# Performance work log

Hardware: AMD Instinct MI355X
Metric: run time of the kernel (lower is better)

The kernel has to match this reference:

```python
import jax, jax.numpy as jnp
import numpy as np

B, T, H, W = 1, 8, 48, 48
EMBED, HEADS = 512, 8
HD = EMBED // HEADS          # 64
KS = 3                       # spatial neighborhood kernel
ROT = HD // 3                # 21 -> 2*(21//2)=20 rotary dims per axis, 60 total
MAX_FREQ = 256.0
EPS = 1e-6


def _rms_norm(x, w):
    return x * jax.lax.rsqrt(jnp.mean(x * x, axis=-1, keepdims=True) + EPS) * w


def _axis_freqs(L, base):
    # freqs_for='pixel': positions in [-1, 1], freqs = linspace(1, max_freq/2)*pi
    pos = jnp.linspace(-1.0, 1.0, L)
    f = pos[:, None] * base[None, :]          # (L, ROT//2)
    return jnp.repeat(f, 2, axis=-1)          # (L, 2*(ROT//2)) interleaved pairs


def _axial_freqs(t, h, w):
    base = jnp.linspace(1.0, MAX_FREQ / 2.0, ROT // 2) * jnp.pi
    ft, fh, fw = _axis_freqs(t, base), _axis_freqs(h, base), _axis_freqs(w, base)
    d = ft.shape[-1]
    ft = jnp.broadcast_to(ft[:, None, None, :], (t, h, w, d))
    fh = jnp.broadcast_to(fh[None, :, None, :], (t, h, w, d))
    fw = jnp.broadcast_to(fw[None, None, :, :], (t, h, w, d))
    return jnp.concatenate([ft, fh, fw], axis=-1)  # (t, h, w, 3*d)


def _rotate_half(x):
    x1, x2 = x[..., ::2], x[..., 1::2]
    return jnp.stack((-x2, x1), axis=-1).reshape(x.shape)


def _apply_rope(freqs, x):
    r = freqs.shape[-1]
    xr, xt = x[..., :r], x[..., r:]
    xr = xr * jnp.cos(freqs) + _rotate_half(xr) * jnp.sin(freqs)
    return jnp.concatenate([xr, xt], axis=-1)


def reference(x, w_qkv, w_out, qnorm_w, knorm_w):
    b, t, h, w, c = x.shape
    # fused QKV: per-head contiguous [q|k|v] chunk of size 3*HD (matches
    # rearrange '(heads head_dim)' with head_dim = 3*HD, then tensor_split(3, -1))
    qkv = (x @ w_qkv.T).reshape(b, t, h, w, HEADS, 3 * HD)
    q, k, v = qkv[..., :HD], qkv[..., HD:2 * HD], qkv[..., 2 * HD:]
    q = _rms_norm(q, qnorm_w)
    k = _rms_norm(k, knorm_w)
    freqs = _axial_freqs(t, h, w)[:, :, :, None, :]  # broadcast over heads
    q = _apply_rope(freqs, q)
    k = _apply_rope(freqs, k)
    # neighborhood attention: full along t, clamped KSxKS window over (h, w)
    ih = jnp.clip(jnp.arange(h) - KS // 2, 0, h - KS)[:, None] + jnp.arange(KS)
    iw = jnp.clip(jnp.arange(w) - KS // 2, 0, w - KS)[:, None] + jnp.arange(KS)
    IH = ih[:, :, None, None]  # (h, KS, 1, 1)
    IW = iw[None, None, :, :]  # (1, 1, w, KS)
    kw = k[:, :, IH, IW]       # (b, t, h, KS, w, KS, heads, HD)
    vw = v[:, :, IH, IW]
    scores = jnp.einsum('btxynd,bsxiyjnd->bntxysij', q, kw) * (HD ** -0.5)
    attn = jax.nn.softmax(scores.reshape(b, HEADS, t, h, w, -1), axis=-1)
    attn = attn.reshape(scores.shape)
    out = jnp.einsum('bntxysij,bsxiyjnd->btxynd', attn, vw)
    out = out.reshape(b, t, h, w, c)
    return out @ w_out.T


def setup_inputs():
    key = jax.random.key(0)
    k1, k2, k3 = jax.random.split(key, 3)
    x = jax.random.normal(k1, (B, T, H, W, EMBED), jnp.float32)
    w_qkv = jax.random.normal(k2, (3 * EMBED, EMBED), jnp.float32) * 0.02
    w_out = jax.random.normal(k3, (EMBED, EMBED), jnp.float32) * 0.02
    qnorm_w = jnp.ones((HD,), jnp.float32)
    knorm_w = jnp.ones((HD,), jnp.float32)
    return dict(x=x, w_qkv=w_qkv, w_out=w_out, qnorm_w=qnorm_w, knorm_w=knorm_w)
```

## Files before the change

kernel.cpp:

```cpp
#include <hip/hip_runtime.h>
#include <hip/hip_bf16.h>
#include <math.h>

#define TOK 18432
#define EMB 512
#define NH 8
#define HD_ 64
#define HH 48
#define WW 48

typedef __attribute__((ext_vector_type(8))) __bf16 bf16x8;
typedef __attribute__((ext_vector_type(4))) float  f32x4;
typedef __attribute__((ext_vector_type(8))) unsigned short u16x8;

__device__ __forceinline__ ushort f2bf(float x) {
    __hip_bfloat16 b = __float2bfloat16(x);
    return *(ushort*)&b;
}
__device__ __forceinline__ float bf2f(ushort u) {
    __hip_bfloat16 b = *(__hip_bfloat16*)&u;
    return __bfloat162float(b);
}

__device__ __forceinline__ void gload16(const void* g, void* l) {
    __builtin_amdgcn_global_load_lds((const __attribute__((address_space(1))) void*)g,
                                     (__attribute__((address_space(3))) void*)l,
                                     16, 0, 0);
}

__device__ __forceinline__ f32x4 mfma_bf16(bf16x8 a, bf16x8 b, f32x4 c) {
    return __builtin_amdgcn_mfma_f32_16x16x32_bf16(a, b, c, 0, 0, 0);
}

__global__ __launch_bounds__(256) void init_misc(const float* __restrict__ x,
                                                 ushort* __restrict__ xhi,
                                                 const float* __restrict__ wq,
                                                 ushort* __restrict__ wqhi,
                                                 const float* __restrict__ wo,
                                                 ushort* __restrict__ wohi,
                                                 float2* __restrict__ tabs) {
    int b = blockIdx.x;
    if (b < 10240) {
        const float* src;
        ushort* dst;
        int i;
        if (b < 9216)      { src = x;  dst = xhi;  i = b * 256 + threadIdx.x; }
        else if (b < 9984) { src = wq; dst = wqhi; i = (b - 9216) * 256 + threadIdx.x; }
        else               { src = wo; dst = wohi; i = (b - 9984) * 256 + threadIdx.x; }
        float4 v = ((const float4*)src)[i];
        ushort4 h = {f2bf(v.x), f2bf(v.y), f2bf(v.z), f2bf(v.w)};
        ((ushort4*)dst)[i] = h;
    } else {
        int idx = (b - 10240) * 256 + threadIdx.x;
        if (idx >= 104 * 10) return;
        int row = idx / 10, j = idx % 10;
        float base = fmaf((float)j, 127.0f / 9.0f, 1.0f) * 3.14159265358979323846f;
        float pos;
        if (row < 8)       pos = fmaf((float)row,        2.0f / 7.0f,  -1.0f);
        else if (row < 56) pos = fmaf((float)(row - 8),  2.0f / 47.0f, -1.0f);
        else               pos = fmaf((float)(row - 56), 2.0f / 47.0f, -1.0f);
        float f = pos * base;
        tabs[idx] = make_float2(cosf(f), sinf(f));
    }
}

__global__ __launch_bounds__(256) void gemm_qkv(const ushort* __restrict__ Ah,
                                                const ushort* __restrict__ Bh,
                                                const float2* __restrict__ tabs,
                                                const float* __restrict__ qnw,
                                                const float* __restrict__ knw,
                                                ushort* __restrict__ qbf,
                                                ushort* __restrict__ kbf,
                                                ushort* __restrict__ vbf) {
    const int K = 512, nM = 12;
    __shared__ __align__(16) char smem[49152];
#define AS_(b) ((ushort*)(smem + (b) * 16384))
#define BS_(b) ((ushort*)(smem + (b) * 16384 + 8192))
    int nwg = gridDim.x;
    int bid = blockIdx.x;
    int cpx = nwg >> 3;
    int swz = (bid & 7) * cpx + (bid >> 3);
    int bm = (swz % nM) * 128, bn = (swz / nM) * 128;
    int tid = threadIdx.x;
    int lane = tid & 63, wave = tid >> 6;
    int wr = wave >> 1, wc = wave & 1;
    int fr = lane & 15, kg = lane >> 4;

    f32x4 acc[4][4];
#pragma unroll
    for (int m = 0; m < 4; ++m)
#pragma unroll
        for (int n = 0; n < 4; ++n) acc[m][n] = (f32x4){0.f, 0.f, 0.f, 0.f};

    auto stage = [&](int buf, int k0) {
#pragma unroll
        for (int it = 0; it < 2; ++it) {
            int f = it * 256 + tid;
            int row = f >> 2, ch = f & 3;
            int sl = ch ^ ((row >> 1) & 3);
            gload16(Ah + (size_t)(bm + row) * K + k0 + sl * 8, AS_(buf) + f * 8);
            gload16(Bh + (size_t)(bn + row) * K + k0 + sl * 8, BS_(buf) + f * 8);
        }
    };

    int nt = K >> 5;
    stage(0, 0);
    int cb = 0, nb = 1;
    int ksw = (kg ^ ((fr >> 1) & 3)) * 8;
    for (int t = 0; t < nt; ++t) {
        if (t + 1 < nt) {
            stage(nb, (t + 1) << 5);
            asm volatile("s_waitcnt vmcnt(4)" ::: "memory");
        } else {
            asm volatile("s_waitcnt vmcnt(0)" ::: "memory");
        }
        __builtin_amdgcn_s_barrier();
        __builtin_amdgcn_sched_barrier(0);
        const ushort* Bc = BS_(cb);
        const ushort* Ac = AS_(cb);
        bf16x8 bh[4];
#pragma unroll
        for (int n = 0; n < 4; ++n)
            bh[n] = *(const bf16x8*)&Bc[(wc * 64 + n * 16 + fr) * 32 + ksw];
#pragma unroll
        for (int m = 0; m < 4; ++m) {
            bf16x8 ah = *(const bf16x8*)&Ac[(wr * 64 + m * 16 + fr) * 32 + ksw];
#pragma unroll
            for (int n = 0; n < 4; ++n)
                acc[m][n] = mfma_bf16(ah, bh[n], acc[m][n]);
        }
        cb = (cb + 1 == 3) ? 0 : cb + 1;
        nb = (nb + 1 == 3) ? 0 : nb + 1;
    }
    __syncthreads();

    int g = (bm >> 6) + wr;
    int type = g % 3;
    int h = g / 3;
    ushort* obuf = (type == 0) ? qbf : (type == 1) ? kbf : vbf;
    float qsc = (type == 0) ? 0.125f : 1.0f;
    float4 wv[4];
    if (type < 2) {
        const float* wptr = type ? knw : qnw;
#pragma unroll
        for (int m = 0; m < 4; ++m)
            wv[m] = *(const float4*)&wptr[m * 16 + kg * 4];
    }
    char* tb = smem + wave * 5120;
    size_t obase = (size_t)h * TOK + bn + wc * 64;

#pragma unroll
    for (int hp = 0; hp < 2; ++hp) {
#pragma unroll
        for (int nn = 0; nn < 2; ++nn) {
            int n = hp * 2 + nn;
            int tk = bn + wc * 64 + n * 16 + fr;
            if (type == 2) {
#pragma unroll
                for (int m = 0; m < 4; ++m) {
                    ushort4 pk = {f2bf(acc[m][n][0]), f2bf(acc[m][n][1]),
                                  f2bf(acc[m][n][2]), f2bf(acc[m][n][3])};
                    *(ushort4*)(tb + (nn * 16 + fr) * 160 + (m * 16 + kg * 4) * 2) = pk;
                }
            } else {
                float s = 0.f;
#pragma unroll
                for (int m = 0; m < 4; ++m)
#pragma unroll
                    for (int i = 0; i < 4; ++i)
                        s = fmaf(acc[m][n][i], acc[m][n][i], s);
                s += __shfl_xor(s, 16);
                s += __shfl_xor(s, 32);
                float inv = rsqrtf(s * (1.0f / 64.0f) + 1e-6f);
                int t = tk / (HH * WW);
                int rem = tk % (HH * WW);
                int xx = rem / WW, yy = rem % WW;
#pragma unroll
                for (int m = 0; m < 4; ++m) {
                    float r[4];
                    const float* wm = (const float*)&wv[m];
#pragma unroll
                    for (int u = 0; u < 2; ++u) {
                        int dc0 = m * 16 + kg * 4 + 2 * u;
                        float xn0 = acc[m][n][2 * u]     * inv * wm[2 * u];
                        float xn1 = acc[m][n][2 * u + 1] * inv * wm[2 * u + 1];
                        if (dc0 < 60) {
                            int p = dc0 >> 1;
                            int tr = (p < 10) ? t * 10 + p
                                   : (p < 20) ? (8 + xx) * 10 + (p - 10)
                                              : (56 + yy) * 10 + (p - 20);
                            float2 cs = tabs[tr];
                            r[2 * u]     = fmaf(xn0, cs.x, -xn1 * cs.y);
                            r[2 * u + 1] = fmaf(xn1, cs.x,  xn0 * cs.y);
                        } else {
                            r[2 * u] = xn0;
                            r[2 * u + 1] = xn1;
                        }
                    }
                    ushort4 pk = {f2bf(r[0] * qsc), f2bf(r[1] * qsc),
                                  f2bf(r[2] * qsc), f2bf(r[3] * qsc)};
                    *(ushort4*)(tb + (nn * 16 + fr) * 160 + (m * 16 + kg * 4) * 2) = pk;
                }
            }
        }
#pragma unroll
        for (int j = 0; j < 4; ++j) {
            int row = j * 8 + (lane >> 3);
            int c16 = (lane & 7) * 16;
            u16x8 v = *(const u16x8*)(tb + row * 160 + c16);
            size_t tok = obase + hp * 32 + row;
            *(u16x8*)(obuf + tok * 64 + (lane & 7) * 8) = v;
        }
    }
#undef AS_
#undef BS_
}

__global__ __launch_bounds__(256) void gemm_out(const ushort* __restrict__ Ah,
                                                const ushort* __restrict__ Bh,
                                                float* __restrict__ C) {
    const int N = 512, K = 512, nbx = 4;
    __shared__ __align__(16) char smem[49152];
#define AS_(b) ((ushort*)(smem + (b) * 16384))
#define BS_(b) ((ushort*)(smem + (b) * 16384 + 8192))
    int nwg = gridDim.x;
    int bid = blockIdx.x;
    int cpx = nwg >> 3;
    int swz = (bid & 7) * cpx + (bid >> 3);
    int bm = (swz / nbx) * 128, bn = (swz % nbx) * 128;
    int tid = threadIdx.x;
    int lane = tid & 63, wave = tid >> 6;
    int wr = wave >> 1, wc = wave & 1;
    int fr = lane & 15, kg = lane >> 4;

    f32x4 acc[4][4];
#pragma unroll
    for (int m = 0; m < 4; ++m)
#pragma unroll
        for (int n = 0; n < 4; ++n) acc[m][n] = (f32x4){0.f, 0.f, 0.f, 0.f};

    auto stage = [&](int buf, int k0) {
#pragma unroll
        for (int it = 0; it < 2; ++it) {
            int f = it * 256 + tid;
            int row = f >> 2, ch = f & 3;
            int sl = ch ^ ((row >> 1) & 3);
            gload16(Ah + (size_t)(bm + row) * K + k0 + sl * 8, AS_(buf) + f * 8);
            gload16(Bh + (size_t)(bn + row) * K + k0 + sl * 8, BS_(buf) + f * 8);
        }
    };

    int nt = K >> 5;
    stage(0, 0);
    int cb = 0, nb = 1;
    int ksw = (kg ^ ((fr >> 1) & 3)) * 8;
    for (int t = 0; t < nt; ++t) {
        if (t + 1 < nt) {
            stage(nb, (t + 1) << 5);
            asm volatile("s_waitcnt vmcnt(4)" ::: "memory");
        } else {
            asm volatile("s_waitcnt vmcnt(0)" ::: "memory");
        }
        __builtin_amdgcn_s_barrier();
        __builtin_amdgcn_sched_barrier(0);
        const ushort* Bc = BS_(cb);
        const ushort* Ac = AS_(cb);
        bf16x8 bh[4];
#pragma unroll
        for (int n = 0; n < 4; ++n)
            bh[n] = *(const bf16x8*)&Bc[(wc * 64 + n * 16 + fr) * 32 + ksw];
#pragma unroll
        for (int m = 0; m < 4; ++m) {
            bf16x8 ah = *(const bf16x8*)&Ac[(wr * 64 + m * 16 + fr) * 32 + ksw];
#pragma unroll
            for (int n = 0; n < 4; ++n)
                acc[m][n] = mfma_bf16(ah, bh[n], acc[m][n]);
        }
        cb = (cb + 1 == 3) ? 0 : cb + 1;
        nb = (nb + 1 == 3) ? 0 : nb + 1;
    }
#pragma unroll
    for (int m = 0; m < 4; ++m) {
        int row0 = bm + wr * 64 + m * 16 + kg * 4;
#pragma unroll
        for (int n = 0; n < 4; ++n) {
            int col = bn + wc * 64 + n * 16 + fr;
#pragma unroll
            for (int i = 0; i < 4; ++i)
                C[(size_t)(row0 + i) * N + col] = acc[m][n][i];
        }
    }
#undef AS_
#undef BS_
}

__global__ __launch_bounds__(256) void attn_mfma(const ushort* __restrict__ qbf,
                                                 const ushort* __restrict__ kbf,
                                                 const ushort* __restrict__ vbf,
                                                 ushort* __restrict__ ohi) {
    __shared__ __align__(16) char smem[45056];
    constexpr int Q_OFF = 0;
    constexpr int K_OFF = 4096;
    constexpr int V_OFF = 20480;
    constexpr int P_OFF = 36864;

    int patch = blockIdx.x, head = blockIdx.y;
    int bi = patch / 24, bj = patch % 24;
    int x0 = bi * 2, y0 = bj * 2;
    int ubx = min(max(x0 - 1, 0), 44), uby = min(max(y0 - 1, 0), 44);
    int tid = threadIdx.x, lane = tid & 63, w = tid >> 6;
    int fr = lane & 15, kg = lane >> 4;
    size_t hbase = (size_t)head * TOK;

    {
        int f = tid;
        int row = f >> 3, sp = f & 7, sl = sp ^ (row & 7);
        int t = row >> 2, px = (row >> 1) & 1, py = row & 1;
        size_t tok = ((size_t)(t * HH + x0 + px)) * WW + (y0 + py);
        gload16(qbf + (hbase + tok) * 64 + sl * 8, smem + Q_OFF + f * 16);
    }
#pragma unroll
    for (int it = 0; it < 4; ++it) {
        int f = it * 256 + tid;
        int row = f >> 3, sp = f & 7, sl = sp ^ (row & 7);
        int s = row >> 4, ki = (row >> 2) & 3, kj = row & 3;
        size_t tok = ((size_t)(s * HH + ubx + ki)) * WW + (uby + kj);
        gload16(kbf + (hbase + tok) * 64 + sl * 8, smem + K_OFF + f * 16);
    }
#pragma unroll
    for (int it = 0; it < 2; ++it) {
        int u = it * 256 + tid;
        int sk = u >> 4, dg = u & 15;
        int s = sk >> 2, ki = sk & 3;
        ushort4 rv[4];
#pragma unroll
        for (int kj = 0; kj < 4; ++kj) {
            size_t tok = ((size_t)(s * HH + ubx + ki)) * WW + (uby + kj);
            rv[kj] = *(const ushort4*)(vbf + (hbase + tok) * 64 + dg * 4);
        }
        const ushort* rr = (const ushort*)rv;
#pragma unroll
        for (int dd = 0; dd < 4; ++dd) {
            int d = dg * 4 + dd;
            ushort4 val = {rr[dd], rr[4 + dd], rr[8 + dd], rr[12 + dd]};
            *(ushort4*)(smem + V_OFF + d * 256 + ((sk * 8) ^ ((d & 7) << 4))) = val;
        }
    }
    __syncthreads();

    if (w < 2) {
        int q = w * 16 + fr;
        bf16x8 qb[2];
#pragma unroll
        for (int ks = 0; ks < 2; ++ks)
            qb[ks] = *(const bf16x8*)(smem + Q_OFF + q * 128 +
                                      ((ks * 64 + kg * 16) ^ ((fr & 7) << 4)));
        f32x4 sc[8];
#pragma unroll
        for (int m = 0; m < 8; ++m) sc[m] = (f32x4){0.f, 0.f, 0.f, 0.f};
#pragma unroll
        for (int m = 0; m < 8; ++m)
#pragma unroll
            for (int ks = 0; ks < 2; ++ks) {
                bf16x8 a = *(const bf16x8*)(smem + K_OFF + (m * 16 + fr) * 128 +
                                            ((ks * 64 + kg * 16) ^ ((fr & 7) << 4)));
                sc[m] = mfma_bf16(a, qb[ks], sc[m]);
            }
        int xq = x0 + ((q >> 1) & 1), yq = y0 + (q & 1);
        int lox = min(max(xq - 1, 0), 45) - ubx;
        int loy = min(max(yq - 1, 0), 45) - uby;
        bool vki = ((unsigned)(kg - lox)) <= 2u;
        float mx = -1e30f;
        if (vki) {
#pragma unroll
            for (int m = 0; m < 8; ++m)
#pragma unroll
                for (int i = 0; i < 4; ++i)
                    if (((unsigned)(i - loy)) <= 2u) mx = fmaxf(mx, sc[m][i]);
        }
        mx = fmaxf(mx, __shfl_xor(mx, 16));
        mx = fmaxf(mx, __shfl_xor(mx, 32));
        float sum = 0.f;
#pragma unroll
        for (int m = 0; m < 8; ++m)
#pragma unroll
            for (int i = 0; i < 4; ++i) {
                bool v = vki && (((unsigned)(i - loy)) <= 2u);
                float e = v ? __expf(sc[m][i] - mx) : 0.f;
                sc[m][i] = e;
                sum += e;
            }
        sum += __shfl_xor(sum, 16);
        sum += __shfl_xor(sum, 32);
        float inv = 1.0f / sum;
#pragma unroll
        for (int m = 0; m < 8; ++m) {
            ushort4 pk = {f2bf(sc[m][0] * inv), f2bf(sc[m][1] * inv),
                          f2bf(sc[m][2] * inv), f2bf(sc[m][3] * inv)};
            *(ushort4*)(smem + P_OFF + q * 256 +
                        ((m * 32 + kg * 8) ^ ((q & 7) << 4))) = pk;
        }
    }
    __syncthreads();

    f32x4 ov[2];
    ov[0] = (f32x4){0.f, 0.f, 0.f, 0.f};
    ov[1] = (f32x4){0.f, 0.f, 0.f, 0.f};
#pragma unroll
    for (int kb = 0; kb < 4; ++kb) {
        bf16x8 a = *(const bf16x8*)(smem + V_OFF + (w * 16 + fr) * 256 +
                                    ((kb * 64 + kg * 16) ^ ((fr & 7) << 4)));
#pragma unroll
        for (int nt2 = 0; nt2 < 2; ++nt2) {
            bf16x8 b = *(const bf16x8*)(smem + P_OFF + (nt2 * 16 + fr) * 256 +
                                        ((kb * 64 + kg * 16) ^ ((fr & 7) << 4)));
            ov[nt2] = mfma_bf16(a, b, ov[nt2]);
        }
    }
#pragma unroll
    for (int nt2 = 0; nt2 < 2; ++nt2) {
        int q = nt2 * 16 + fr;
        int t = q >> 2, px = (q >> 1) & 1, py = q & 1;
        size_t tok = ((size_t)(t * HH + x0 + px)) * WW + (y0 + py);
        size_t ob = tok * 512 + head * 64 + w * 16 + kg * 4;
        ushort4 hv = {f2bf(ov[nt2][0]), f2bf(ov[nt2][1]),
                      f2bf(ov[nt2][2]), f2bf(ov[nt2][3])};
        *(ushort4*)&ohi[ob] = hv;
    }
}

extern "C" void kernel_launch(void* const* d_in, const int* in_sizes, int n_in,
                              void* d_out, int out_size, void* d_ws, size_t ws_size,
                              hipStream_t stream) {
    const float* x     = (const float*)d_in[0];
    const float* w_qkv = (const float*)d_in[1];
    const float* w_out = (const float*)d_in[2];
    const float* qnw   = (const float*)d_in[3];
    const float* knw   = (const float*)d_in[4];
    float* out = (float*)d_out;
    char*  ws  = (char*)d_ws;

    const size_t TABS_B = 16384;
    const size_t WQ_B   = (size_t)1536 * 512 * 2;
    const size_t WO_B   = (size_t)512 * 512 * 2;

    float2* tabs = (float2*)ws;
    ushort* wqhi = (ushort*)(ws + TABS_B);
    ushort* wohi = wqhi + (size_t)1536 * 512;
    ushort* qbf  = (ushort*)(ws + TABS_B + WQ_B + WO_B);
    ushort* kbf  = qbf + (size_t)TOK * 512;
    ushort* vbf  = kbf + (size_t)TOK * 512;
    ushort* ohi  = vbf + (size_t)TOK * 512;

    ushort* xhi = (ushort*)d_out;

    init_misc<<<10245, 256, 0, stream>>>(x, xhi, w_qkv, wqhi, w_out, wohi, tabs);

    gemm_qkv<<<(1536 / 128) * (TOK / 128), 256, 0, stream>>>(
        wqhi, xhi, tabs, qnw, knw, qbf, kbf, vbf);
    attn_mfma<<<dim3(576, NH), 256, 0, stream>>>(qbf, kbf, vbf, ohi);
    gemm_out<<<(TOK / 128) * (512 / 128), 256, 0, stream>>>(ohi, wohi, out);
}
```

Baseline: 104.4 us.

## Split attention score/softmax across all four waves with shared-memory max/sum reduction

The QK^T scoring and softmax stage used to run on only two of the four waves, leaving the other two idle. Each query tile's 128 keys are now split into two halves handled by separate waves. Partial row max and row sum are exchanged through small shared-memory buffers, which costs two extra block-wide barriers. The MFMA loops are also wrapped in s_setprio to raise wave priority while they run.

```diff
diff --git a/kernel.cpp b/kernel.cpp
--- a/kernel.cpp
+++ b/kernel.cpp
@@ -298,11 +298,13 @@
                                                  const ushort* __restrict__ kbf,
                                                  const ushort* __restrict__ vbf,
                                                  ushort* __restrict__ ohi) {
-    __shared__ __align__(16) char smem[45056];
+    __shared__ __align__(16) char smem[45568];
     constexpr int Q_OFF = 0;
     constexpr int K_OFF = 4096;
     constexpr int V_OFF = 20480;
     constexpr int P_OFF = 36864;
+    constexpr int XM_OFF = 45056;
+    constexpr int XS_OFF = 45312;
 
     int patch = blockIdx.x, head = blockIdx.y;
     int bi = patch / 24, bj = patch % 24;
@@ -348,24 +350,31 @@
     }
     __syncthreads();
 
-    if (w < 2) {
-        int q = w * 16 + fr;
+    float* XM = (float*)(smem + XM_OFF);
+    float* XS = (float*)(smem + XS_OFF);
+    int qt = w & 1, mh = w >> 1;
+    int q = qt * 16 + fr;
+    {
         bf16x8 qb[2];
 #pragma unroll
         for (int ks = 0; ks < 2; ++ks)
             qb[ks] = *(const bf16x8*)(smem + Q_OFF + q * 128 +
                                       ((ks * 64 + kg * 16) ^ ((fr & 7) << 4)));
-        f32x4 sc[8];
-#pragma unroll
-        for (int m = 0; m < 8; ++m) sc[m] = (f32x4){0.f, 0.f, 0.f, 0.f};
-#pragma unroll
-        for (int m = 0; m < 8; ++m)
+        f32x4 sc[4];
+#pragma unroll
+        for (int mm = 0; mm < 4; ++mm) sc[mm] = (f32x4){0.f, 0.f, 0.f, 0.f};
+        __builtin_amdgcn_s_setprio(1);
+#pragma unroll
+        for (int mm = 0; mm < 4; ++mm) {
+            int m = mh * 4 + mm;
 #pragma unroll
             for (int ks = 0; ks < 2; ++ks) {
                 bf16x8 a = *(const bf16x8*)(smem + K_OFF + (m * 16 + fr) * 128 +
                                             ((ks * 64 + kg * 16) ^ ((fr & 7) << 4)));
-                sc[m] = mfma_bf16(a, qb[ks], sc[m]);
+                sc[mm] = mfma_bf16(a, qb[ks], sc[mm]);
             }
+        }
+        __builtin_amdgcn_s_setprio(0);
         int xq = x0 + ((q >> 1) & 1), yq = y0 + (q & 1);
         int lox = min(max(xq - 1, 0), 45) - ubx;
         int loy = min(max(yq - 1, 0), 45) - uby;
@@ -373,30 +382,36 @@
         float mx = -1e30f;
         if (vki) {
 #pragma unroll
-            for (int m = 0; m < 8; ++m)
+            for (int mm = 0; mm < 4; ++mm)
 #pragma unroll
                 for (int i = 0; i < 4; ++i)
-                    if (((unsigned)(i - loy)) <= 2u) mx = fmaxf(mx, sc[m][i]);
+                    if (((unsigned)(i - loy)) <= 2u) mx = fmaxf(mx, sc[mm][i]);
         }
         mx = fmaxf(mx, __shfl_xor(mx, 16));
         mx = fmaxf(mx, __shfl_xor(mx, 32));
+        if (kg == 0) XM[(qt * 2 + mh) * 16 + fr] = mx;
+        __syncthreads();
+        mx = fmaxf(XM[(qt * 2 + 0) * 16 + fr], XM[(qt * 2 + 1) * 16 + fr]);
         float sum = 0.f;
 #pragma unroll
-        for (int m = 0; m < 8; ++m)
+        for (int mm = 0; mm < 4; ++mm)
 #pragma unroll
             for (int i = 0; i < 4; ++i) {
                 bool v = vki && (((unsigned)(i - loy)) <= 2u);
-                float e = v ? __expf(sc[m][i] - mx) : 0.f;
-                sc[m][i] = e;
+                float e = v ? __expf(sc[mm][i] - mx) : 0.f;
+                sc[mm][i] = e;
                 sum += e;
             }
         sum += __shfl_xor(sum, 16);
         sum += __shfl_xor(sum, 32);
-        float inv = 1.0f / sum;
-#pragma unroll
-        for (int m = 0; m < 8; ++m) {
-            ushort4 pk = {f2bf(sc[m][0] * inv), f2bf(sc[m][1] * inv),
-                          f2bf(sc[m][2] * inv), f2bf(sc[m][3] * inv)};
+        if (kg == 0) XS[(qt * 2 + mh) * 16 + fr] = sum;
+        __syncthreads();
+        float inv = 1.0f / (XS[(qt * 2 + 0) * 16 + fr] + XS[(qt * 2 + 1) * 16 + fr]);
+#pragma unroll
+        for (int mm = 0; mm < 4; ++mm) {
+            int m = mh * 4 + mm;
+            ushort4 pk = {f2bf(sc[mm][0] * inv), f2bf(sc[mm][1] * inv),
+                          f2bf(sc[mm][2] * inv), f2bf(sc[mm][3] * inv)};
             *(ushort4*)(smem + P_OFF + q * 256 +
                         ((m * 32 + kg * 8) ^ ((q & 7) << 4))) = pk;
         }
@@ -406,6 +421,7 @@
     f32x4 ov[2];
     ov[0] = (f32x4){0.f, 0.f, 0.f, 0.f};
     ov[1] = (f32x4){0.f, 0.f, 0.f, 0.f};
+    __builtin_amdgcn_s_setprio(1);
 #pragma unroll
     for (int kb = 0; kb < 4; ++kb) {
         bf16x8 a = *(const bf16x8*)(smem + V_OFF + (w * 16 + fr) * 256 +
@@ -417,10 +433,11 @@
             ov[nt2] = mfma_bf16(a, b, ov[nt2]);
         }
     }
+    __builtin_amdgcn_s_setprio(0);
 #pragma unroll
     for (int nt2 = 0; nt2 < 2; ++nt2) {
-        int q = nt2 * 16 + fr;
-        int t = q >> 2, px = (q >> 1) & 1, py = q & 1;
+        int qq = nt2 * 16 + fr;
+        int t = qq >> 2, px = (qq >> 1) & 1, py = qq & 1;
         size_t tok = ((size_t)(t * HH + x0 + px)) * WW + (y0 + py);
         size_t ob = tok * 512 + head * 64 + w * 16 + kg * 4;
         ushort4 hv = {f2bf(ov[nt2][0]), f2bf(ov[nt2][1]),
```

Measured after the change: 103.0 us. Within noise of the previous version (-1.3%).
